# Kernel tuning notes

Hardware: AMD Instinct MI355X
Metric: run time of the kernel (lower is better)

## Reference

```python
import jax, jax.numpy as jnp
import numpy as np

M_CONST = 0.05  # monotonicity margin m from __init__ default


def setup_inputs() -> dict:
    key = jax.random.key(0)
    ks = jax.random.split(key, 5)
    B, IN, OUT = 262144, 128, 128
    scale = 1.0 / np.sqrt(IN)
    return {
        "x": jax.random.normal(ks[0], (B, IN), dtype=jnp.float32),
        "z": jax.random.normal(ks[1], (B, OUT), dtype=jnp.float32),
        "U_w": jax.random.normal(ks[2], (OUT, IN), dtype=jnp.float32) * scale,
        "U_b": jax.random.normal(ks[3], (OUT,), dtype=jnp.float32) * scale,
        "A_w": jax.random.normal(ks[4], (OUT, OUT), dtype=jnp.float32) * scale,
        "d": jnp.zeros((OUT,), dtype=jnp.float32),
    }


def reference(x, z, U_w, U_b, A_w, d):
    # U(x) = x @ U_w.T + U_b
    ux = x @ U_w.T + U_b
    # rowSums diag: diag(|A| @ 1) -> per-output-row abs row sums; z @ diag(r) = z * r
    row_sums = jnp.sum(jnp.abs(A_w), axis=1)  # [OUT]
    dw = jnp.exp(d)                            # diag weights
    # transformedA = diag(1/dw) @ A @ diag(dw); z @ transformedA.T = ((z*dw) @ A.T) * (1/dw)
    z_lin = ((z * dw) @ A_w.T) / dw
    z_out = M_CONST * z + z_lin - z * row_sums
    return (ux + z_out,)
```

## Files before the change

### kernel.cpp

```cpp
#include <hip/hip_runtime.h>
#include <hip/hip_bf16.h>

typedef __attribute__((ext_vector_type(8)))  float f8;
typedef __attribute__((ext_vector_type(16))) float f32x16;
typedef __attribute__((ext_vector_type(8)))  short bf8;

__device__ __forceinline__ short f2bf(float f) {
    unsigned u = __builtin_bit_cast(unsigned, f);
    u += 0x7fff + ((u >> 16) & 1);
    return (short)(u >> 16);
}

__device__ __forceinline__ unsigned cvt_pk_bf16(float a, float b) {
    unsigned r;
    asm("v_cvt_pk_bf16_f32 %0, %1, %2" : "=v"(r) : "v"(a), "v"(b));
    return r;
}

__global__ void nemon_prep(const float* __restrict__ Uw,
                           const float* __restrict__ Aw,
                           const float* __restrict__ dvec,
                           short* __restrict__ pre)
{
    __shared__ float rs[128], dwv[128];
    const int tid = threadIdx.x;
    if (tid < 128) {
        float s = 0.f;
        #pragma unroll 8
        for (int k = 0; k < 128; ++k) s += fabsf(Aw[tid * 128 + k]);
        rs[tid]  = s;
        dwv[tid] = expf(dvec[tid]);
    }
    __syncthreads();
    #pragma unroll
    for (int half = 0; half < 2; ++half) {
        const int e    = blockIdx.x * 512 + half * 256 + tid;
        const int j    = e & 7;
        const int lane = (e >> 3) & 63;
        const int f    = e >> 9;
        const int nt   = f & 3;
        const int kt   = f >> 2;
        const int k    = kt * 16 + (lane >> 5) * 8 + j;
        const int n    = nt * 32 + (lane & 31);
        float v;
        if (k < 128) {
            v = Uw[n * 128 + k];
        } else {
            const int k2 = k - 128;
            v = Aw[n * 128 + k2] * (dwv[k2] / dwv[n]);
            if (n == k2) v += 0.05f - rs[n];
        }
        pre[e] = f2bf(v);
    }
}

__global__ __launch_bounds__(256, 4) void nemon_main(
    const float* __restrict__ x,
    const float* __restrict__ z,
    const float* __restrict__ Ub,
    const short* __restrict__ pre,
    float* __restrict__ out)
{
    const int tid  = threadIdx.x;
    const int wave = tid >> 6;
    const int lane = tid & 63;
    const int lo   = lane & 31;
    const int hi   = lane >> 5;

    const long R = ((long)blockIdx.x * 4 + wave) * 32;

    f32x16 acc[4];
    #pragma unroll
    for (int nt = 0; nt < 4; ++nt) {
        const float b = Ub[nt * 32 + lo];
        #pragma unroll
        for (int r = 0; r < 16; ++r) acc[nt][r] = b;
    }

    const float* xr = x + (R + lo) * 128 + hi * 8;
    const float* zr = z + (R + lo) * 128 + hi * 8;

    #pragma unroll
    for (int kt = 0; kt < 16; ++kt) {
        const float* src = (kt < 8) ? (xr + kt * 16) : (zr + (kt - 8) * 16);
        f8 v = *(const f8*)src;
        union { bf8 b; unsigned u[4]; } a;
        a.u[0] = cvt_pk_bf16(v[0], v[1]);
        a.u[1] = cvt_pk_bf16(v[2], v[3]);
        a.u[2] = cvt_pk_bf16(v[4], v[5]);
        a.u[3] = cvt_pk_bf16(v[6], v[7]);
        #pragma unroll
        for (int nt = 0; nt < 4; ++nt) {
            bf8 b = *(const bf8*)(pre + (long)((kt * 4 + nt) * 64 + lane) * 8);
            acc[nt] = __builtin_amdgcn_mfma_f32_32x32x16_bf16(a.b, b, acc[nt], 0, 0, 0);
        }
    }

    float* ob = out + R * 128;
    #pragma unroll
    for (int reg = 0; reg < 16; ++reg) {
        const int rowA = (reg & 3) + 8 * (reg >> 2) + 4 * hi;
        #pragma unroll
        for (int nt = 0; nt < 4; ++nt)
            ob[rowA * 128 + nt * 32 + lo] = acc[nt][reg];
    }
}

extern "C" void kernel_launch(void* const* d_in, const int* in_sizes, int n_in,
                              void* d_out, int out_size, void* d_ws, size_t ws_size,
                              hipStream_t stream) {
    const float* x  = (const float*)d_in[0];
    const float* z  = (const float*)d_in[1];
    const float* Uw = (const float*)d_in[2];
    const float* Ub = (const float*)d_in[3];
    const float* Aw = (const float*)d_in[4];
    const float* dv = (const float*)d_in[5];
    float* out = (float*)d_out;
    short* pre = (short*)d_ws;

    const int B = in_sizes[0] / 128;
    nemon_prep<<<64, 256, 0, stream>>>(Uw, Aw, dv, pre);
    nemon_main<<<B / 128, 256, 0, stream>>>(x, z, Ub, pre, out);
}
```

Baseline: 113.3 us.

## Split output columns across waves and preload all inputs into registers

Each block now handles 32 rows, and each of its four waves computes one 32-column output tile instead of one wave owning all 128 columns. The wave's B fragments and all of its x/z rows are loaded into registers up front, so memory loads can overlap before the MFMA chain starts. The four waves of a block read the same x/z rows, which rely on cache for reuse, and the grid becomes four times larger. Launch bounds are relaxed to allow more registers per thread.

```diff
diff --git a/kernel.cpp b/kernel.cpp
--- a/kernel.cpp
+++ b/kernel.cpp
@@ -54,7 +54,7 @@
     }
 }
 
-__global__ __launch_bounds__(256, 4) void nemon_main(
+__global__ __launch_bounds__(256, 1) void nemon_main(
     const float* __restrict__ x,
     const float* __restrict__ z,
     const float* __restrict__ Ub,
@@ -67,42 +67,52 @@
     const int lo   = lane & 31;
     const int hi   = lane >> 5;
 
-    const long R = ((long)blockIdx.x * 4 + wave) * 32;
+    const long R = (long)blockIdx.x * 32;
 
-    f32x16 acc[4];
+    bf8 w[16];
     #pragma unroll
-    for (int nt = 0; nt < 4; ++nt) {
-        const float b = Ub[nt * 32 + lo];
-        #pragma unroll
-        for (int r = 0; r < 16; ++r) acc[nt][r] = b;
-    }
+    for (int kt = 0; kt < 16; ++kt)
+        w[kt] = *(const bf8*)(pre + (long)((kt * 4 + wave) * 64 + lane) * 8);
 
     const float* xr = x + (R + lo) * 128 + hi * 8;
     const float* zr = z + (R + lo) * 128 + hi * 8;
+    f8 xv[8], zv[8];
+    #pragma unroll
+    for (int i = 0; i < 8; ++i) xv[i] = *(const f8*)(xr + i * 16);
+    #pragma unroll
+    for (int i = 0; i < 8; ++i) zv[i] = *(const f8*)(zr + i * 16);
+
+    f32x16 acc;
+    {
+        const float b = Ub[wave * 32 + lo];
+        #pragma unroll
+        for (int r = 0; r < 16; ++r) acc[r] = b;
+    }
 
     #pragma unroll
-    for (int kt = 0; kt < 16; ++kt) {
-        const float* src = (kt < 8) ? (xr + kt * 16) : (zr + (kt - 8) * 16);
-        f8 v = *(const f8*)src;
+    for (int kt = 0; kt < 8; ++kt) {
         union { bf8 b; unsigned u[4]; } a;
-        a.u[0] = cvt_pk_bf16(v[0], v[1]);
-        a.u[1] = cvt_pk_bf16(v[2], v[3]);
-        a.u[2] = cvt_pk_bf16(v[4], v[5]);
-        a.u[3] = cvt_pk_bf16(v[6], v[7]);
-        #pragma unroll
-        for (int nt = 0; nt < 4; ++nt) {
-            bf8 b = *(const bf8*)(pre + (long)((kt * 4 + nt) * 64 + lane) * 8);
-            acc[nt] = __builtin_amdgcn_mfma_f32_32x32x16_bf16(a.b, b, acc[nt], 0, 0, 0);
-        }
+        a.u[0] = cvt_pk_bf16(xv[kt][0], xv[kt][1]);
+        a.u[1] = cvt_pk_bf16(xv[kt][2], xv[kt][3]);
+        a.u[2] = cvt_pk_bf16(xv[kt][4], xv[kt][5]);
+        a.u[3] = cvt_pk_bf16(xv[kt][6], xv[kt][7]);
+        acc = __builtin_amdgcn_mfma_f32_32x32x16_bf16(a.b, w[kt], acc, 0, 0, 0);
+    }
+    #pragma unroll
+    for (int kt = 0; kt < 8; ++kt) {
+        union { bf8 b; unsigned u[4]; } a;
+        a.u[0] = cvt_pk_bf16(zv[kt][0], zv[kt][1]);
+        a.u[1] = cvt_pk_bf16(zv[kt][2], zv[kt][3]);
+        a.u[2] = cvt_pk_bf16(zv[kt][4], zv[kt][5]);
+        a.u[3] = cvt_pk_bf16(zv[kt][6], zv[kt][7]);
+        acc = __builtin_amdgcn_mfma_f32_32x32x16_bf16(a.b, w[kt + 8], acc, 0, 0, 0);
     }
 
-    float* ob = out + R * 128;
+    float* ob = out + R * 128 + wave * 32 + lo;
     #pragma unroll
     for (int reg = 0; reg < 16; ++reg) {
         const int rowA = (reg & 3) + 8 * (reg >> 2) + 4 * hi;
-        #pragma unroll
-        for (int nt = 0; nt < 4; ++nt)
-            ob[rowA * 128 + nt * 32 + lo] = acc[nt][reg];
+        ob[rowA * 128] = acc[reg];
     }
 }
 
@@ -120,5 +130,5 @@
 
     const int B = in_sizes[0] / 128;
     nemon_prep<<<64, 256, 0, stream>>>(Uw, Aw, dv, pre);
-    nemon_main<<<B / 128, 256, 0, stream>>>(x, z, Ub, pre, out);
+    nemon_main<<<B / 32, 256, 0, stream>>>(x, z, Ub, pre, out);
 }
```

New measurement: 160.9 us. +42.0%, slower.
